# Optimization experiments

Measured on AMD Instinct MI355X. Metric: run time of the kernel, lower is better.

## Reference

```python
import jax, jax.numpy as jnp
import numpy as np

D_MODEL = 512
N_HEADS = 8
D_K = 64
D_V = 64
SEQ = 2048
BATCH = 4
WINDOW = 256  # mask_lenth
LN_EPS = 1e-5


def setup_inputs() -> dict:
    key = jax.random.key(0)
    ks = jax.random.split(key, 7)
    s = 1.0 / np.sqrt(D_MODEL)
    return {
        "input_Q": jax.random.normal(ks[0], (BATCH, SEQ, D_MODEL), jnp.float32),
        "input_K": jax.random.normal(ks[1], (BATCH, SEQ, D_MODEL), jnp.float32),
        "input_V": jax.random.normal(ks[2], (BATCH, SEQ, D_MODEL), jnp.float32),
        "W_Q": jax.random.normal(ks[3], (D_MODEL, N_HEADS * D_K), jnp.float32) * s,
        "W_K": jax.random.normal(ks[4], (D_MODEL, N_HEADS * D_K), jnp.float32) * s,
        "W_V": jax.random.normal(ks[5], (D_MODEL, N_HEADS * D_V), jnp.float32) * s,
        "W_fc": jax.random.normal(ks[6], (N_HEADS * D_V, D_MODEL), jnp.float32) * s,
    }


def _band_mask(n, w):
    # keep entries with i-(w-1) <= j <= i  (lower band of width w incl. diagonal)
    i = jnp.arange(n)[:, None]
    j = jnp.arange(n)[None, :]
    return (j <= i) & (j >= i - (w - 1))


def reference(input_Q, input_K, input_V, W_Q, W_K, W_V, W_fc):
    B, L, _ = input_Q.shape
    # projections -> [B, H, L, d]
    Q = (input_Q @ W_Q).reshape(B, L, N_HEADS, D_K).transpose(0, 2, 1, 3)
    K = (input_K @ W_K).reshape(B, L, N_HEADS, D_K).transpose(0, 2, 1, 3)
    V = (input_V @ W_V).reshape(B, L, N_HEADS, D_V).transpose(0, 2, 1, 3)

    scores = jnp.einsum("bhqd,bhkd->bhqk", Q, K) / np.sqrt(D_K)
    mask = _band_mask(L, WINDOW)  # [L, L] bool
    scores = jnp.where(mask[None, None], scores, -jnp.inf)
    attn = jax.nn.softmax(scores, axis=-1)
    context = jnp.einsum("bhqk,bhkd->bhqd", attn, V)  # [B,H,L,d_v]
    context = context.transpose(0, 2, 1, 3).reshape(B, L, N_HEADS * D_V)
    out = context @ W_fc + input_Q  # residual
    # LayerNorm (fresh nn.LayerNorm: gamma=1, beta=0)
    mu = jnp.mean(out, axis=-1, keepdims=True)
    var = jnp.var(out, axis=-1, keepdims=True)
    return (out - mu) * jax.lax.rsqrt(var + LN_EPS)
```

## Files before the change

kernel.cpp:

```cpp
#include <hip/hip_runtime.h>
#include <hip/hip_bf16.h>

#define D_MODEL 512
#define NH      8
#define SEQ     2048
#define BATCH   4
#define WINDOW  256
#define ROWS    (BATCH*SEQ)

typedef __attribute__((ext_vector_type(8))) short bf16x8;
typedef __attribute__((ext_vector_type(4))) float f32x4;
typedef __hip_bfloat16 bf16;

__device__ __forceinline__ f32x4 mfma16(bf16x8 a, bf16x8 b, f32x4 c) {
    return __builtin_amdgcn_mfma_f32_16x16x32_bf16(a, b, c, 0, 0, 0);
}

__device__ __forceinline__ void gload16(const void* g, void* l) {
    __builtin_amdgcn_global_load_lds((const __attribute__((address_space(1))) void*)g,
                                     (__attribute__((address_space(3))) void*)l, 16, 0, 0);
}

__device__ __forceinline__ unsigned pack2(float lo, float hi) {
    float2 t; t.x = lo; t.y = hi;
    __hip_bfloat162 h = __float22bfloat162_rn(t);
    return *(unsigned*)&h;
}

__global__ __launch_bounds__(256)
void wconv(const float* __restrict__ W0, const float* __restrict__ W1,
           const float* __restrict__ W2, const float* __restrict__ W3,
           bf16* __restrict__ Wt) {
    const int z = blockIdx.z;
    const float* W = (z == 0) ? W0 : (z == 1) ? W1 : (z == 2) ? W2 : W3;
    bf16* dst = Wt + (size_t)z * D_MODEL * D_MODEL;

    __shared__ float t[64][65];
    const int k0 = blockIdx.x * 64, n0 = blockIdx.y * 64;
    const int tid = threadIdx.x;

    #pragma unroll
    for (int i = 0; i < 16; ++i) {
        const int e = tid + 256 * i, r = e >> 6, c = e & 63;
        t[r][c] = W[(size_t)(k0 + r) * D_MODEL + n0 + c];
    }
    __syncthreads();
    #pragma unroll
    for (int i = 0; i < 16; ++i) {
        const int e = tid + 256 * i, r = e >> 6, c = e & 63;
        dst[(size_t)(n0 + r) * D_MODEL + k0 + c] = __float2bfloat16(t[c][r]);
    }
}

__global__ __launch_bounds__(512)
void proj_mfma(const float* __restrict__ Xq, const float* __restrict__ Xk,
               const float* __restrict__ Xv, const bf16* __restrict__ Wt,
               bf16* __restrict__ Qp, bf16* __restrict__ Kp, bf16* __restrict__ Vp) {
    const int z = blockIdx.z;
    const float* X = (z == 0) ? Xq : (z == 1) ? Xk : Xv;
    const bf16* W = Wt + (size_t)z * D_MODEL * D_MODEL;
    bf16* outp = (z == 0) ? Qp : (z == 1) ? Kp : Vp;

    __shared__ bf16 Asw[2][128 * 32];
    __shared__ bf16 Bsw[2][128 * 32];

    const int tid = threadIdx.x;
    const int lane = tid & 63, w = tid >> 6;
    const int wr = w >> 2, wc = w & 3;
    const int row0 = blockIdx.x * 128, col0 = blockIdx.y * 128;
    const int g = lane >> 4, m16 = lane & 15;

    f32x4 acc[4][2] = {};
    float4 a0, a1;

    auto stageB = [&](int buf, int k0) {
        const int n = tid >> 2, s = tid & 3;
        gload16(W + (size_t)(col0 + n) * D_MODEL + k0 + ((s ^ (n & 3)) * 8),
                &Bsw[buf][tid * 8]);
    };
    auto loadA = [&](int k0) {
        const int m = tid >> 2, s = tid & 3;
        const float* gp = X + (size_t)(row0 + m) * D_MODEL + k0 + ((s ^ (m & 3)) * 8);
        a0 = *(const float4*)gp;
        a1 = *(const float4*)(gp + 4);
    };
    auto writeA = [&](int buf) {
        const int m = tid >> 2, s = tid & 3;
        int4 pk;
        pk.x = pack2(a0.x, a0.y);
        pk.y = pack2(a0.z, a0.w);
        pk.z = pack2(a1.x, a1.y);
        pk.w = pack2(a1.z, a1.w);
        *(int4*)&Asw[buf][m * 32 + s * 8] = pk;
    };

    stageB(0, 0);
    loadA(0);
    writeA(0);
    __syncthreads();

    int cur = 0;
    for (int step = 0; step < 16; ++step) {
        const int k0n = (step + 1) * 32;
        if (step < 15) { stageB(cur ^ 1, k0n); loadA(k0n); }

        bf16x8 af[4], bfr[2];
        #pragma unroll
        for (int mi = 0; mi < 4; ++mi) {
            const int m = wr * 64 + mi * 16 + m16;
            af[mi] = *(const bf16x8*)&Asw[cur][m * 32 + ((g ^ (m & 3)) * 8)];
        }
        #pragma unroll
        for (int ni = 0; ni < 2; ++ni) {
            const int n = wc * 32 + ni * 16 + m16;
            bfr[ni] = *(const bf16x8*)&Bsw[cur][n * 32 + ((g ^ (n & 3)) * 8)];
        }
        #pragma unroll
        for (int mi = 0; mi < 4; ++mi)
            #pragma unroll
            for (int ni = 0; ni < 2; ++ni)
                acc[mi][ni] = mfma16(af[mi], bfr[ni], acc[mi][ni]);

        if (step < 15) {
            writeA(cur ^ 1);
            __syncthreads();
        }
        cur ^= 1;
    }

    if (z < 2) {
        #pragma unroll
        for (int mi = 0; mi < 4; ++mi)
            #pragma unroll
            for (int ni = 0; ni < 2; ++ni) {
                const int c = col0 + wc * 32 + ni * 16 + m16;
                const int h = c >> 6, d = c & 63;
                #pragma unroll
                for (int reg = 0; reg < 4; ++reg) {
                    const int r = row0 + wr * 64 + mi * 16 + g * 4 + reg;
                    const int b = r >> 11, l = r & (SEQ - 1);
                    outp[(((size_t)b * NH + h) * SEQ + l) * 64 + d] =
                        __float2bfloat16(acc[mi][ni][reg]);
                }
            }
    } else {
        #pragma unroll
        for (int mi = 0; mi < 4; ++mi)
            #pragma unroll
            for (int ni = 0; ni < 2; ++ni) {
                const int c = col0 + wc * 32 + ni * 16 + m16;
                const int h = c >> 6, d = c & 63;
                const int r = row0 + wr * 64 + mi * 16 + g * 4;
                const int b = r >> 11, l = r & (SEQ - 1);
                uint2 pv;
                pv.x = pack2(acc[mi][ni][0], acc[mi][ni][1]);
                pv.y = pack2(acc[mi][ni][2], acc[mi][ni][3]);
                *(uint2*)&outp[(((size_t)b * NH + h) * 64 + d) * SEQ + l] = pv;
            }
    }
}

__global__ __launch_bounds__(256)
void attn_mfma(const bf16* __restrict__ Qp, const bf16* __restrict__ Kp,
               const bf16* __restrict__ Vp, bf16* __restrict__ ctx) {
    __shared__ bf16 QP[64 * 64];
    __shared__ bf16 Ks[2][64 * 64];
    __shared__ bf16 Vt[2][64 * 64];

    const int bh = blockIdx.y, b = bh >> 3, h = bh & 7;
    const int q0 = blockIdx.x * 64;
    const int tid = threadIdx.x;
    const int lane = tid & 63, w = tid >> 6;
    const int g = lane >> 4, m16 = lane & 15;

    const size_t kvbase = (size_t)bh * SEQ * 64;
    const size_t vtbase = (size_t)bh * 64 * SEQ;

    auto stageKV = [&](int buf, int k0) {
        #pragma unroll
        for (int i = 0; i < 2; ++i) {
            const int chunk = i * 256 + tid;
            const int r = chunk >> 3, s = chunk & 7;
            gload16(Kp + kvbase + (size_t)(k0 + r) * 64 + ((s ^ (r & 7)) * 8),
                    &Ks[buf][(i * 256 + w * 64) * 8]);
            gload16(Vp + vtbase + (size_t)r * SEQ + k0 + ((s ^ (r & 7)) * 8),
                    &Vt[buf][(i * 256 + w * 64) * 8]);
        }
    };

    int klo = q0 - (WINDOW - 1); if (klo < 0) klo = 0;
    const int kt0 = klo >> 6, kt1 = q0 >> 6;

    #pragma unroll
    for (int i = 0; i < 2; ++i) {
        const int chunk = i * 256 + tid;
        const int r = chunk >> 3, s = chunk & 7;
        gload16(Qp + kvbase + (size_t)(q0 + r) * 64 + ((s ^ (r & 7)) * 8),
                &QP[(i * 256 + w * 64) * 8]);
    }
    stageKV(0, kt0 * 64);
    __syncthreads();

    bf16x8 qf[2];
    #pragma unroll
    for (int c = 0; c < 2; ++c) {
        const int r = w * 16 + m16;
        qf[c] = *(const bf16x8*)&QP[r * 64 + (((c * 4 + g) ^ (m16 & 7)) * 8)];
    }

    f32x4 o[4] = {};
    float rs = 0.f;
    const int qg = q0 + w * 16 + m16;

    int cur = 0;
    for (int kt = kt0; kt <= kt1; ++kt) {
        const int k0 = kt * 64;
        if (kt < kt1) stageKV(cur ^ 1, (kt + 1) * 64);

        f32x4 st[4] = {};
        #pragma unroll
        for (int c = 0; c < 2; ++c) {
            bf16x8 kf[4];
            #pragma unroll
            for (int f = 0; f < 4; ++f) {
                const int r = f * 16 + m16;
                kf[f] = *(const bf16x8*)&Ks[cur][r * 64 + (((c * 4 + g) ^ (m16 & 7)) * 8)];
            }
            #pragma unroll
            for (int f = 0; f < 4; ++f)
                st[f] = mfma16(kf[f], qf[c], st[f]);
        }

        const int masktype = (k0 == q0) ? 1 : ((k0 < q0 - 192) ? 2 : 0);
        #pragma unroll
        for (int f = 0; f < 4; ++f) {
            float p[4];
            #pragma unroll
            for (int reg = 0; reg < 4; ++reg) {
                const int kg = k0 + f * 16 + g * 4 + reg;
                bool valid = (masktype == 0) || (masktype == 1 ? (kg <= qg)
                                                              : (kg >= qg - (WINDOW - 1)));
                p[reg] = valid ? __expf(st[f][reg] * 0.125f) : 0.f;
                rs += p[reg];
            }
            uint2 pkv;
            pkv.x = pack2(p[0], p[1]);
            pkv.y = pack2(p[2], p[3]);
            const int slot = (f * 2 + (g >> 1)) ^ (m16 & 7);
            *(uint2*)&QP[w * 1024 + m16 * 64 + slot * 8 + (g & 1) * 4] = pkv;
        }

        #pragma unroll
        for (int c = 0; c < 2; ++c) {
            const bf16x8 pf =
                *(const bf16x8*)&QP[w * 1024 + m16 * 64 + (((c * 4 + g) ^ (m16 & 7)) * 8)];
            #pragma unroll
            for (int f2 = 0; f2 < 4; ++f2) {
                const int r = f2 * 16 + m16;
                const bf16x8 vf =
                    *(const bf16x8*)&Vt[cur][r * 64 + (((c * 4 + g) ^ (m16 & 7)) * 8)];
                o[f2] = mfma16(pf, vf, o[f2]);
            }
        }

        if (kt < kt1) __syncthreads();
        cur ^= 1;
    }

    rs += __shfl_xor(rs, 16, 64);
    rs += __shfl_xor(rs, 32, 64);
    const float inv = 1.0f / rs;
    float invr[4];
    #pragma unroll
    for (int reg = 0; reg < 4; ++reg)
        invr[reg] = __shfl(inv, g * 4 + reg, 64);

    #pragma unroll
    for (int f2 = 0; f2 < 4; ++f2) {
        const int d = f2 * 16 + m16;
        #pragma unroll
        for (int reg = 0; reg < 4; ++reg) {
            const int qrow = w * 16 + g * 4 + reg;
            ctx[((size_t)b * SEQ + q0 + qrow) * D_MODEL + h * 64 + d] =
                __float2bfloat16(o[f2][reg] * invr[reg]);
        }
    }
}

__global__ __launch_bounds__(512)
void fc_mfma(const bf16* __restrict__ ctx, const bf16* __restrict__ Wt,
             const float* __restrict__ resid, float* __restrict__ out) {
    __shared__ bf16 Asw[2][128 * 32];
    __shared__ bf16 Bsw[2][128 * 32];

    const int tid = threadIdx.x;
    const int lane = tid & 63, w = tid >> 6;
    const int wr = w >> 2, wc = w & 3;
    const int row0 = blockIdx.x * 128, col0 = blockIdx.y * 128;
    const int g = lane >> 4, m16 = lane & 15;

    f32x4 acc[4][2] = {};

    auto stage = [&](int buf, int k0) {
        const int m = tid >> 2, s = tid & 3;
        gload16(ctx + (size_t)(row0 + m) * D_MODEL + k0 + ((s ^ (m & 3)) * 8),
                &Asw[buf][tid * 8]);
        gload16(Wt + (size_t)(col0 + m) * D_MODEL + k0 + ((s ^ (m & 3)) * 8),
                &Bsw[buf][tid * 8]);
    };

    stage(0, 0);
    __syncthreads();

    int cur = 0;
    for (int step = 0; step < 16; ++step) {
        if (step < 15) stage(cur ^ 1, (step + 1) * 32);

        bf16x8 af[4], bfr[2];
        #pragma unroll
        for (int mi = 0; mi < 4; ++mi) {
            const int m = wr * 64 + mi * 16 + m16;
            af[mi] = *(const bf16x8*)&Asw[cur][m * 32 + ((g ^ (m & 3)) * 8)];
        }
        #pragma unroll
        for (int ni = 0; ni < 2; ++ni) {
            const int n = wc * 32 + ni * 16 + m16;
            bfr[ni] = *(const bf16x8*)&Bsw[cur][n * 32 + ((g ^ (n & 3)) * 8)];
        }
        #pragma unroll
        for (int mi = 0; mi < 4; ++mi)
            #pragma unroll
            for (int ni = 0; ni < 2; ++ni)
                acc[mi][ni] = mfma16(af[mi], bfr[ni], acc[mi][ni]);

        if (step < 15) __syncthreads();
        cur ^= 1;
    }

    #pragma unroll
    for (int mi = 0; mi < 4; ++mi)
        #pragma unroll
        for (int ni = 0; ni < 2; ++ni) {
            const int c = col0 + wc * 32 + ni * 16 + m16;
            #pragma unroll
            for (int reg = 0; reg < 4; ++reg) {
                const int r = row0 + wr * 64 + mi * 16 + g * 4 + reg;
                out[(size_t)r * D_MODEL + c] = acc[mi][ni][reg] + resid[(size_t)r * D_MODEL + c];
            }
        }
}

__global__ __launch_bounds__(256)
void ln_kernel(float* __restrict__ out) {
    const int row = blockIdx.x;
    float* p = out + (size_t)row * D_MODEL;
    const int tid = threadIdx.x;

    float2 x = *(float2*)&p[tid * 2];
    float s  = x.x + x.y;
    float s2 = x.x * x.x + x.y * x.y;
    #pragma unroll
    for (int m = 1; m < 64; m <<= 1) {
        s  += __shfl_xor(s,  m, 64);
        s2 += __shfl_xor(s2, m, 64);
    }
    __shared__ float sa[4], sb[4];
    const int w = tid >> 6;
    if ((tid & 63) == 0) { sa[w] = s; sb[w] = s2; }
    __syncthreads();
    s  = sa[0] + sa[1] + sa[2] + sa[3];
    s2 = sb[0] + sb[1] + sb[2] + sb[3];

    const float mean = s * (1.0f / D_MODEL);
    const float var  = s2 * (1.0f / D_MODEL) - mean * mean;
    const float rstd = rsqrtf(var + 1e-5f);

    x.x = (x.x - mean) * rstd;
    x.y = (x.y - mean) * rstd;
    *(float2*)&p[tid * 2] = x;
}

extern "C" void kernel_launch(void* const* d_in, const int* in_sizes, int n_in,
                              void* d_out, int out_size, void* d_ws, size_t ws_size,
                              hipStream_t stream) {
    const float* inQ = (const float*)d_in[0];
    const float* inK = (const float*)d_in[1];
    const float* inV = (const float*)d_in[2];
    const float* WQ  = (const float*)d_in[3];
    const float* WK  = (const float*)d_in[4];
    const float* WV  = (const float*)d_in[5];
    const float* Wfc = (const float*)d_in[6];
    float* out = (float*)d_out;

    bf16* ws = (bf16*)d_ws;
    const size_t WSZ = (size_t)D_MODEL * D_MODEL;
    const size_t NE  = (size_t)BATCH * NH * SEQ * 64;
    bf16* Wt   = ws;
    bf16* Qp   = ws + 4 * WSZ;
    bf16* Kp   = Qp + NE;
    bf16* Vp   = Kp + NE;
    bf16* ctxb = Vp + NE;

    wconv<<<dim3(8, 8, 4), 256, 0, stream>>>(WQ, WK, WV, Wfc, Wt);
    proj_mfma<<<dim3(ROWS / 128, D_MODEL / 128, 3), 512, 0, stream>>>(
        inQ, inK, inV, Wt, Qp, Kp, Vp);
    attn_mfma<<<dim3(SEQ / 64, BATCH * NH), 256, 0, stream>>>(Qp, Kp, Vp, ctxb);
    fc_mfma<<<dim3(ROWS / 128, D_MODEL / 128), 512, 0, stream>>>(
        ctxb, Wt + 3 * WSZ, inQ, out);
    ln_kernel<<<ROWS, 256, 0, stream>>>(out);
}
```

Baseline: 168.9 us.

## Pre-convert inputs to bf16 and triple-buffer GEMM loads with async LDS staging

```diff
diff --git a/kernel.cpp b/kernel.cpp
--- a/kernel.cpp
+++ b/kernel.cpp
@@ -25,6 +25,24 @@
     float2 t; t.x = lo; t.y = hi;
     __hip_bfloat162 h = __float22bfloat162_rn(t);
     return *(unsigned*)&h;
+}
+
+__global__ __launch_bounds__(256)
+void xconv(const float* __restrict__ Xq, const float* __restrict__ Xk,
+           const float* __restrict__ Xv, bf16* __restrict__ Xb) {
+    const int z = blockIdx.y;
+    const float* src = (z == 0) ? Xq : (z == 1) ? Xk : Xv;
+    bf16* dst = Xb + (size_t)z * ROWS * D_MODEL;
+
+    const int idx = blockIdx.x * 256 + threadIdx.x;
+    const float4 f0 = ((const float4*)src)[idx * 2];
+    const float4 f1 = ((const float4*)src)[idx * 2 + 1];
+    int4 pk;
+    pk.x = pack2(f0.x, f0.y);
+    pk.y = pack2(f0.z, f0.w);
+    pk.z = pack2(f1.x, f1.y);
+    pk.w = pack2(f1.z, f1.w);
+    ((int4*)dst)[idx] = pk;
 }
 
 __global__ __launch_bounds__(256)
@@ -53,16 +71,15 @@
 }
 
 __global__ __launch_bounds__(512)
-void proj_mfma(const float* __restrict__ Xq, const float* __restrict__ Xk,
-               const float* __restrict__ Xv, const bf16* __restrict__ Wt,
+void proj_mfma(const bf16* __restrict__ Xb, const bf16* __restrict__ Wt,
                bf16* __restrict__ Qp, bf16* __restrict__ Kp, bf16* __restrict__ Vp) {
     const int z = blockIdx.z;
-    const float* X = (z == 0) ? Xq : (z == 1) ? Xk : Xv;
+    const bf16* X = Xb + (size_t)z * ROWS * D_MODEL;
     const bf16* W = Wt + (size_t)z * D_MODEL * D_MODEL;
     bf16* outp = (z == 0) ? Qp : (z == 1) ? Kp : Vp;
 
-    __shared__ bf16 Asw[2][128 * 32];
-    __shared__ bf16 Bsw[2][128 * 32];
+    __shared__ bf16 As[3][128 * 32];
+    __shared__ bf16 Bs[3][128 * 32];
 
     const int tid = threadIdx.x;
     const int lane = tid & 63, w = tid >> 6;
@@ -71,62 +88,54 @@
     const int g = lane >> 4, m16 = lane & 15;
 
     f32x4 acc[4][2] = {};
-    float4 a0, a1;
-
-    auto stageB = [&](int buf, int k0) {
-        const int n = tid >> 2, s = tid & 3;
-        gload16(W + (size_t)(col0 + n) * D_MODEL + k0 + ((s ^ (n & 3)) * 8),
-                &Bsw[buf][tid * 8]);
+
+    const int sn = tid >> 2, ss = tid & 3;
+    const int soff = (ss ^ ((sn >> 1) & 3)) * 8;
+
+    auto stage = [&](int buf, int t) {
+        const int k0 = t * 32;
+        gload16(X + (size_t)(row0 + sn) * D_MODEL + k0 + soff, &As[buf][tid * 8]);
+        gload16(W + (size_t)(col0 + sn) * D_MODEL + k0 + soff, &Bs[buf][tid * 8]);
     };
-    auto loadA = [&](int k0) {
-        const int m = tid >> 2, s = tid & 3;
-        const float* gp = X + (size_t)(row0 + m) * D_MODEL + k0 + ((s ^ (m & 3)) * 8);
-        a0 = *(const float4*)gp;
-        a1 = *(const float4*)(gp + 4);
-    };
-    auto writeA = [&](int buf) {
-        const int m = tid >> 2, s = tid & 3;
-        int4 pk;
-        pk.x = pack2(a0.x, a0.y);
-        pk.y = pack2(a0.z, a0.w);
-        pk.z = pack2(a1.x, a1.y);
-        pk.w = pack2(a1.z, a1.w);
-        *(int4*)&Asw[buf][m * 32 + s * 8] = pk;
-    };
-
-    stageB(0, 0);
-    loadA(0);
-    writeA(0);
-    __syncthreads();
-
-    int cur = 0;
-    for (int step = 0; step < 16; ++step) {
-        const int k0n = (step + 1) * 32;
-        if (step < 15) { stageB(cur ^ 1, k0n); loadA(k0n); }
-
+    auto compute = [&](int buf) {
         bf16x8 af[4], bfr[2];
         #pragma unroll
         for (int mi = 0; mi < 4; ++mi) {
             const int m = wr * 64 + mi * 16 + m16;
-            af[mi] = *(const bf16x8*)&Asw[cur][m * 32 + ((g ^ (m & 3)) * 8)];
+            af[mi] = *(const bf16x8*)&As[buf][m * 32 + ((g ^ ((m >> 1) & 3)) * 8)];
         }
         #pragma unroll
         for (int ni = 0; ni < 2; ++ni) {
             const int n = wc * 32 + ni * 16 + m16;
-            bfr[ni] = *(const bf16x8*)&Bsw[cur][n * 32 + ((g ^ (n & 3)) * 8)];
+            bfr[ni] = *(const bf16x8*)&Bs[buf][n * 32 + ((g ^ ((n >> 1) & 3)) * 8)];
         }
         #pragma unroll
         for (int mi = 0; mi < 4; ++mi)
             #pragma unroll
             for (int ni = 0; ni < 2; ++ni)
                 acc[mi][ni] = mfma16(af[mi], bfr[ni], acc[mi][ni]);
-
-        if (step < 15) {
-            writeA(cur ^ 1);
-            __syncthreads();
-        }
-        cur ^= 1;
-    }
+    };
+
+    stage(0, 0);
+    stage(1, 1);
+
+    int ib = 0;
+    #pragma unroll 1
+    for (int t = 0; t < 15; ++t) {
+        asm volatile("s_waitcnt vmcnt(2)" ::: "memory");
+        __builtin_amdgcn_s_barrier();
+        __builtin_amdgcn_sched_barrier(0);
+        if (t + 2 < 16) {
+            const int nb = (ib + 2 >= 3) ? ib - 1 : ib + 2;
+            stage(nb, t + 2);
+        }
+        compute(ib);
+        ib = (ib + 1 == 3) ? 0 : ib + 1;
+    }
+    asm volatile("s_waitcnt vmcnt(0)" ::: "memory");
+    __builtin_amdgcn_s_barrier();
+    __builtin_amdgcn_sched_barrier(0);
+    compute(ib);
 
     if (z < 2) {
         #pragma unroll
@@ -290,8 +299,8 @@
 __global__ __launch_bounds__(512)
 void fc_mfma(const bf16* __restrict__ ctx, const bf16* __restrict__ Wt,
              const float* __restrict__ resid, float* __restrict__ out) {
-    __shared__ bf16 Asw[2][128 * 32];
-    __shared__ bf16 Bsw[2][128 * 32];
+    __shared__ bf16 As[3][128 * 32];
+    __shared__ bf16 Bs[3][128 * 32];
 
     const int tid = threadIdx.x;
     const int lane = tid & 63, w = tid >> 6;
@@ -301,41 +310,53 @@
 
     f32x4 acc[4][2] = {};
 
-    auto stage = [&](int buf, int k0) {
-        const int m = tid >> 2, s = tid & 3;
-        gload16(ctx + (size_t)(row0 + m) * D_MODEL + k0 + ((s ^ (m & 3)) * 8),
-                &Asw[buf][tid * 8]);
-        gload16(Wt + (size_t)(col0 + m) * D_MODEL + k0 + ((s ^ (m & 3)) * 8),
-                &Bsw[buf][tid * 8]);
+    const int sn = tid >> 2, ss = tid & 3;
+    const int soff = (ss ^ ((sn >> 1) & 3)) * 8;
+
+    auto stage = [&](int buf, int t) {
+        const int k0 = t * 32;
+        gload16(ctx + (size_t)(row0 + sn) * D_MODEL + k0 + soff, &As[buf][tid * 8]);
+        gload16(Wt + (size_t)(col0 + sn) * D_MODEL + k0 + soff, &Bs[buf][tid * 8]);
     };
-
-    stage(0, 0);
-    __syncthreads();
-
-    int cur = 0;
-    for (int step = 0; step < 16; ++step) {
-        if (step < 15) stage(cur ^ 1, (step + 1) * 32);
-
+    auto compute = [&](int buf) {
         bf16x8 af[4], bfr[2];
         #pragma unroll
         for (int mi = 0; mi < 4; ++mi) {
             const int m = wr * 64 + mi * 16 + m16;
-            af[mi] = *(const bf16x8*)&Asw[cur][m * 32 + ((g ^ (m & 3)) * 8)];
+            af[mi] = *(const bf16x8*)&As[buf][m * 32 + ((g ^ ((m >> 1) & 3)) * 8)];
         }
         #pragma unroll
         for (int ni = 0; ni < 2; ++ni) {
             const int n = wc * 32 + ni * 16 + m16;
-            bfr[ni] = *(const bf16x8*)&Bsw[cur][n * 32 + ((g ^ (n & 3)) * 8)];
+            bfr[ni] = *(const bf16x8*)&Bs[buf][n * 32 + ((g ^ ((n >> 1) & 3)) * 8)];
         }
         #pragma unroll
         for (int mi = 0; mi < 4; ++mi)
             #pragma unroll
             for (int ni = 0; ni < 2; ++ni)
                 acc[mi][ni] = mfma16(af[mi], bfr[ni], acc[mi][ni]);
-
-        if (step < 15) __syncthreads();
-        cur ^= 1;
-    }
+    };
+
+    stage(0, 0);
+    stage(1, 1);
+
+    int ib = 0;
+    #pragma unroll 1
+    for (int t = 0; t < 15; ++t) {
+        asm volatile("s_waitcnt vmcnt(2)" ::: "memory");
+        __builtin_amdgcn_s_barrier();
+        __builtin_amdgcn_sched_barrier(0);
+        if (t + 2 < 16) {
+            const int nb = (ib + 2 >= 3) ? ib - 1 : ib + 2;
+            stage(nb, t + 2);
+        }
+        compute(ib);
+        ib = (ib + 1 == 3) ? 0 : ib + 1;
+    }
+    asm volatile("s_waitcnt vmcnt(0)" ::: "memory");
+    __builtin_amdgcn_s_barrier();
+    __builtin_amdgcn_sched_barrier(0);
+    compute(ib);
 
     #pragma unroll
     for (int mi = 0; mi < 4; ++mi)
@@ -396,14 +417,16 @@
     const size_t WSZ = (size_t)D_MODEL * D_MODEL;
     const size_t NE  = (size_t)BATCH * NH * SEQ * 64;
     bf16* Wt   = ws;
-    bf16* Qp   = ws + 4 * WSZ;
+    bf16* Xb   = ws + 4 * WSZ;
+    bf16* Qp   = Xb + 3 * NE;
     bf16* Kp   = Qp + NE;
     bf16* Vp   = Kp + NE;
     bf16* ctxb = Vp + NE;
 
+    xconv<<<dim3(ROWS * D_MODEL / (256 * 8), 3), 256, 0, stream>>>(inQ, inK, inV, Xb);
     wconv<<<dim3(8, 8, 4), 256, 0, stream>>>(WQ, WK, WV, Wfc, Wt);
     proj_mfma<<<dim3(ROWS / 128, D_MODEL / 128, 3), 512, 0, stream>>>(
-        inQ, inK, inV, Wt, Qp, Kp, Vp);
+        Xb, Wt, Qp, Kp, Vp);
     attn_mfma<<<dim3(SEQ / 64, BATCH * NH), 256, 0, stream>>>(Qp, Kp, Vp, ctxb);
     fc_mfma<<<dim3(ROWS / 128, D_MODEL / 128), 512, 0, stream>>>(
         ctxb, Wt + 3 * WSZ, inQ, out);
```

New measurement: 165.8 us. No clear change (-1.8%).
